# Kernel optimization log

Measured on AMD Instinct MI355X. Metric: run time of the kernel, lower is better.

The kernel has to match this reference:

```python
import jax, jax.numpy as jnp
import numpy as np

N_NODES = 100000
N_EDGES = 1600000
IN_DIM, HID_DIM, OUT_DIM = 256, 64, 64
EPS = 1e-12  # F.normalize eps


def _gcn_conv(x, src, dst, norm, W, b, num_nodes):
    # PyG-style GCNConv: transform, then symmetric-normalized aggregation.
    h = x @ W                                   # [N, d_out]
    msg = norm[:, None] * h[src]                # [E+N, d_out] gathered messages
    out = jax.ops.segment_sum(msg, dst, num_segments=num_nodes)
    return out + b


def _l2_normalize(h):
    # F.normalize(h, p=2, dim=1)
    n = jnp.sqrt(jnp.sum(h * h, axis=-1, keepdims=True))
    return h / jnp.maximum(n, EPS)


def setup_inputs() -> dict:
    key = jax.random.key(0)
    ks = jax.random.split(key, 8)
    x = jax.random.normal(ks[0], (N_NODES, IN_DIM), dtype=jnp.float32)
    edge_index = jax.random.randint(ks[1], (2, N_EDGES), 0, N_NODES, dtype=jnp.int64)
    def glorot(k, fan_in, fan_out):
        s = np.sqrt(6.0 / (fan_in + fan_out)).astype(np.float32)
        return jax.random.uniform(k, (fan_in, fan_out), jnp.float32, -s, s)
    W1 = glorot(ks[2], IN_DIM, HID_DIM)
    W2 = glorot(ks[3], HID_DIM, HID_DIM)
    W3 = glorot(ks[4], HID_DIM, OUT_DIM)
    b1 = jnp.zeros((HID_DIM,), jnp.float32)
    b2 = jnp.zeros((HID_DIM,), jnp.float32)
    b3 = jnp.zeros((OUT_DIM,), jnp.float32)
    return {"x": x, "edge_index": edge_index,
            "W1": W1, "b1": b1, "W2": W2, "b2": b2, "W3": W3, "b3": b3}


def reference(x, edge_index, W1, b1, W2, b2, W3, b3):
    N = x.shape[0]
    # add self-loops and compute symmetric norm D^-1/2 A_hat D^-1/2
    loop = jnp.arange(N, dtype=edge_index.dtype)
    src = jnp.concatenate([edge_index[0], loop])
    dst = jnp.concatenate([edge_index[1], loop])
    deg = jax.ops.segment_sum(jnp.ones_like(src, dtype=x.dtype), dst, num_segments=N)
    dinv = jnp.where(deg > 0, jax.lax.rsqrt(jnp.maximum(deg, 1.0)), 0.0)
    norm = dinv[src] * dinv[dst]                # [E+N]

    # layer 1: conv -> relu -> (dropout p=0 = identity) -> L2-normalize
    h = jax.nn.relu(_gcn_conv(x, src, dst, norm, W1, b1, N))
    h = _l2_normalize(h)
    # layer 2
    h = jax.nn.relu(_gcn_conv(h, src, dst, norm, W2, b2, N))
    h = _l2_normalize(h)
    # final layer: plain conv (cast to float32, already float32)
    out = _gcn_conv(h, src, dst, norm, W3, b3, N)
    return out
```

## Files before the change

kernel.cpp:

```cpp
#include <hip/hip_runtime.h>
#include <hip/hip_bf16.h>
#include <math.h>

#define HID 64
#define KT 64

#define NBBITS 10
#define NBSZ 1024
#define P1_BMAX 128
#define P1_CH 4096
#define P1_CAP 96

static inline size_t align256(size_t x) { return (x + 255) & ~(size_t)255; }

__device__ inline void gld_lds16(const float* g, float* lds) {
  __builtin_amdgcn_global_load_lds((const __attribute__((address_space(1))) void*)g,
                                   (__attribute__((address_space(3))) void*)lds, 16, 0, 0);
}


__global__ void count_dst_kernel(const int* __restrict__ dst, int* __restrict__ cnt, int E) {
  int e = blockIdx.x * blockDim.x + threadIdx.x;
  if (e < E) atomicAdd(&cnt[dst[e]], 1);
}

__global__ void dinv_kernel(const int* __restrict__ cnt, float* __restrict__ dinv, int N) {
  int i = blockIdx.x * blockDim.x + threadIdx.x;
  if (i < N) dinv[i] = rsqrtf((float)(cnt[i] + 1));
}


__global__ void bucket_count_kernel(const int* __restrict__ dst, int* __restrict__ bcnt,
                                    int E, int B) {
  __shared__ int sh[1024];
  for (int i = threadIdx.x; i < B; i += blockDim.x) sh[i] = 0;
  __syncthreads();
  for (int e = blockIdx.x * blockDim.x + threadIdx.x; e < E; e += gridDim.x * blockDim.x)
    atomicAdd(&sh[dst[e] >> NBBITS], 1);
  __syncthreads();
  for (int i = threadIdx.x; i < B; i += blockDim.x) {
    int v = sh[i];
    if (v) atomicAdd(&bcnt[i], v);
  }
}

__global__ __launch_bounds__(1024) void bucket_scan_kernel(const int* __restrict__ bcnt,
                                                           int* __restrict__ bbase,
                                                           int* __restrict__ gcur, int B) {
  __shared__ int sh[1024];
  int t = threadIdx.x;
  int v = (t < B) ? bcnt[t] : 0;
  sh[t] = v;
  __syncthreads();
  for (int off = 1; off < 1024; off <<= 1) {
    int u = (t >= off) ? sh[t - off] : 0;
    __syncthreads();
    sh[t] += u;
    __syncthreads();
  }
  if (t < B) {
    int ex = sh[t] - v;
    bbase[t] = ex;
    gcur[t] = ex;
  }
  if (t == 1023) bbase[B] = sh[1023];
}

__global__ __launch_bounds__(256) void bucketize_kernel(const int* __restrict__ src,
                                                        const int* __restrict__ dst,
                                                        int* __restrict__ gcur,
                                                        int* __restrict__ ebuck, int E) {
  __shared__ int cnt[P1_BMAX];
  __shared__ int lists[P1_BMAX * P1_CAP];
  int t = threadIdx.x;
  for (int i = t; i < P1_BMAX; i += 256) cnt[i] = 0;
  __syncthreads();
  int base_e = blockIdx.x * P1_CH;
#pragma unroll
  for (int u = 0; u < P1_CH / 256; ++u) {
    int e = base_e + u * 256 + t;
    if (e < E) {
      int s = src[e], d = dst[e];
      int bk = d >> NBBITS;
      int packed = (s << NBBITS) | (d & (NBSZ - 1));
      int p = atomicAdd(&cnt[bk], 1);
      if (p < P1_CAP) {
        lists[bk * P1_CAP + p] = packed;
      } else {
        int gp = atomicAdd(&gcur[bk], 1);
        ebuck[gp] = packed;
      }
    }
  }
  __syncthreads();
  int w = t >> 6, lane = t & 63;
  int bk = w * 32 + (lane & 31);
  int c = min(cnt[bk], P1_CAP);
  int mybase = 0;
  if (lane < 32 && c > 0) mybase = atomicAdd(&gcur[bk], c);
#pragma unroll 1
  for (int i = 0; i < 32; ++i) {
    int cb = __shfl(c, i);
    if (cb == 0) continue;
    int gb = __shfl(mybase, i);
    int bb = w * 32 + i;
    if (lane < cb) ebuck[gb + lane] = lists[bb * P1_CAP + lane];
    if (cb > 64 && lane < cb - 64) ebuck[gb + 64 + lane] = lists[bb * P1_CAP + 64 + lane];
  }
}

__global__ __launch_bounds__(1024) void bucket_sort_kernel(const int* __restrict__ ebuck,
                                                           const int* __restrict__ bbase,
                                                           int* __restrict__ rowptr,
                                                           int* __restrict__ epack,
                                                           int N, int B, int E) {
  __shared__ int lcnt[NBSZ];
  __shared__ int lcur[NBSZ];
  int b = blockIdx.x;
  int t = threadIdx.x;
  int n0 = b << NBBITS;
  lcnt[t] = 0;
  __syncthreads();
  int e0 = bbase[b], e1 = bbase[b + 1];
  for (int i = e0 + t; i < e1; i += 1024) atomicAdd(&lcnt[ebuck[i] & (NBSZ - 1)], 1);
  __syncthreads();
  int v = lcnt[t];
  for (int off = 1; off < 1024; off <<= 1) {
    int u = (t >= off) ? lcnt[t - off] : 0;
    __syncthreads();
    lcnt[t] += u;
    __syncthreads();
  }
  int ex = lcnt[t] - v;
  int node = n0 + t;
  if (node < N) rowptr[node] = e0 + ex;
  if (b == B - 1 && t == 0) rowptr[N] = E;
  lcur[t] = e0 + ex;
  __syncthreads();
  for (int i = e0 + t; i < e1; i += 1024) {
    int pv = ebuck[i];
    int pos = atomicAdd(&lcur[pv & (NBSZ - 1)], 1);
    epack[pos] = ((unsigned)pv) >> NBBITS;
  }
}

__global__ void dinv_rowptr_kernel(const int* __restrict__ rowptr, float* __restrict__ dinv,
                                   int N) {
  int i = blockIdx.x * blockDim.x + threadIdx.x;
  if (i < N) dinv[i] = rsqrtf((float)(rowptr[i + 1] - rowptr[i] + 1));
}


template <int K, typename OT>
__global__ __launch_bounds__(256, 4) void gemm_kernel(const float* __restrict__ x,
                                                      const float* __restrict__ W,
                                                      OT* __restrict__ out, int N) {
  __shared__ float Xs[64 * KT];
  __shared__ float Ws[KT * 64];
  const int t = threadIdx.x;
  const int lane = t & 63;
  const int w = t >> 6;
  const int rg = lane >> 4;
  const int cg = lane & 15;
  const int row0 = blockIdx.x * 64;
  float4 acc[4];
#pragma unroll
  for (int r = 0; r < 4; ++r) acc[r] = make_float4(0.f, 0.f, 0.f, 0.f);

  for (int k0 = 0; k0 < K; k0 += KT) {
    if (k0) __syncthreads();
    const float* Wg = W + (size_t)k0 * HID;
#pragma unroll
    for (int c = 0; c < 4; ++c) {
      int idx = c * 256 + t;
      gld_lds16(Wg + idx * 4, &Ws[idx * 4]);
      int srow = idx >> 4;
      int sg = (idx & 15) ^ ((srow >> 2) & 3);
      int grow = min(row0 + srow, N - 1);
      gld_lds16(x + (size_t)grow * K + k0 + (sg << 2), &Xs[idx * 4]);
    }
    __syncthreads();
    const int rbase = w * 16 + rg * 4;
#pragma unroll 4
    for (int kb = 0; kb < KT / 4; ++kb) {
      float4 wq0 = *(const float4*)&Ws[(4 * kb + 0) * HID + cg * 4];
      float4 wq1 = *(const float4*)&Ws[(4 * kb + 1) * HID + cg * 4];
      float4 wq2 = *(const float4*)&Ws[(4 * kb + 2) * HID + cg * 4];
      float4 wq3 = *(const float4*)&Ws[(4 * kb + 3) * HID + cg * 4];
      const int sg = (kb ^ rg) << 2;
#pragma unroll
      for (int r = 0; r < 4; ++r) {
        float4 xv = *(const float4*)&Xs[(rbase + r) * KT + sg];
        acc[r].x = fmaf(xv.w, wq3.x, fmaf(xv.z, wq2.x, fmaf(xv.y, wq1.x, fmaf(xv.x, wq0.x, acc[r].x))));
        acc[r].y = fmaf(xv.w, wq3.y, fmaf(xv.z, wq2.y, fmaf(xv.y, wq1.y, fmaf(xv.x, wq0.y, acc[r].y))));
        acc[r].z = fmaf(xv.w, wq3.z, fmaf(xv.z, wq2.z, fmaf(xv.y, wq1.z, fmaf(xv.x, wq0.z, acc[r].z))));
        acc[r].w = fmaf(xv.w, wq3.w, fmaf(xv.z, wq2.w, fmaf(xv.y, wq1.w, fmaf(xv.x, wq0.w, acc[r].w))));
      }
    }
  }
#pragma unroll
  for (int r = 0; r < 4; ++r) {
    int row = row0 + w * 16 + rg * 4 + r;
    if (row < N) {
      OT* o = out + (size_t)row * HID + cg * 4;
      o[0] = (OT)acc[r].x; o[1] = (OT)acc[r].y; o[2] = (OT)acc[r].z; o[3] = (OT)acc[r].w;
    }
  }
}


__device__ inline float bf_lo(unsigned int u) { return __uint_as_float(u << 16); }
__device__ inline float bf_hi(unsigned int u) { return __uint_as_float(u & 0xffff0000u); }

template <bool RELU_NORM>
__global__ void agg_kernel(const int* __restrict__ rowptr, const int* __restrict__ ep,
                           const float* __restrict__ dinv, const uint2* __restrict__ h64,
                           const float* __restrict__ bias, float* __restrict__ out, int N) {
  int grp = (blockIdx.x * blockDim.x + threadIdx.x) >> 6;
  int lane = threadIdx.x & 63;
  int q = lane >> 4;
  int sub = lane & 15;
  int node = grp * 4 + q;
  if (node >= N) return;
  int beg = rowptr[node];
  int end = rowptr[node + 1];
  float di = dinv[node];
  float dd = di * di;
  uint2 su = h64[(size_t)node * 16 + sub];
  float4 b4 = *(const float4*)&bias[sub * 4];
  float a0 = dd * bf_lo(su.x) + b4.x;
  float a1 = dd * bf_hi(su.x) + b4.y;
  float a2 = dd * bf_lo(su.y) + b4.z;
  float a3 = dd * bf_hi(su.y) + b4.w;
  int j = beg;
  for (; j + 8 <= end; j += 8) {
    int e[8];
    float dv[8];
    uint2 hv[8];
#pragma unroll
    for (int u = 0; u < 8; ++u) e[u] = ep[j + u];
#pragma unroll
    for (int u = 0; u < 8; ++u) dv[u] = dinv[e[u]];
#pragma unroll
    for (int u = 0; u < 8; ++u) hv[u] = h64[(size_t)e[u] * 16 + sub];
#pragma unroll
    for (int u = 0; u < 8; ++u) {
      float wn = di * dv[u];
      a0 = fmaf(wn, bf_lo(hv[u].x), a0);
      a1 = fmaf(wn, bf_hi(hv[u].x), a1);
      a2 = fmaf(wn, bf_lo(hv[u].y), a2);
      a3 = fmaf(wn, bf_hi(hv[u].y), a3);
    }
  }
  for (; j < end; ++j) {
    int e0 = ep[j];
    float wn = di * dinv[e0];
    uint2 hu = h64[(size_t)e0 * 16 + sub];
    a0 = fmaf(wn, bf_lo(hu.x), a0);
    a1 = fmaf(wn, bf_hi(hu.x), a1);
    a2 = fmaf(wn, bf_lo(hu.y), a2);
    a3 = fmaf(wn, bf_hi(hu.y), a3);
  }
  float4 v;
  if (RELU_NORM) {
    v.x = fmaxf(a0, 0.f); v.y = fmaxf(a1, 0.f);
    v.z = fmaxf(a2, 0.f); v.w = fmaxf(a3, 0.f);
    float ss = v.x * v.x + v.y * v.y + v.z * v.z + v.w * v.w;
#pragma unroll
    for (int off = 8; off; off >>= 1) ss += __shfl_xor(ss, off, 64);
    float inv = 1.f / fmaxf(sqrtf(ss), 1e-12f);
    v.x *= inv; v.y *= inv; v.z *= inv; v.w *= inv;
  } else {
    v = make_float4(a0, a1, a2, a3);
  }
  *(float4*)&out[(size_t)node * HID + sub * 4] = v;
}


__global__ void init_agg_kernel(const float* __restrict__ dinv, const float* __restrict__ h,
                                const float* __restrict__ bias, float* __restrict__ out, int N) {
  int t = blockIdx.x * blockDim.x + threadIdx.x;
  int i = t >> 6, f = t & 63;
  if (i >= N) return;
  float di = dinv[i];
  out[t] = di * di * h[t] + bias[f];
}

__global__ void edge_atomic_kernel(const int* __restrict__ src, const int* __restrict__ dst,
                                   const float* __restrict__ dinv, const float* __restrict__ h,
                                   float* __restrict__ out, int E) {
  int t = blockIdx.x * blockDim.x + threadIdx.x;
  int e = t >> 6;
  if (e >= E) return;
  int f = t & 63;
  int s = src[e], d = dst[e];
  atomicAdd(&out[(size_t)d * HID + f], dinv[s] * dinv[d] * h[(size_t)s * HID + f]);
}

__global__ void relu_norm_kernel(float* __restrict__ hbuf, int N) {
  int t = blockIdx.x * blockDim.x + threadIdx.x;
  int i = t >> 6;
  if (i >= N) return;
  float v = fmaxf(hbuf[t], 0.f);
  float ss = v * v;
#pragma unroll
  for (int off = 32; off; off >>= 1) ss += __shfl_xor(ss, off, 64);
  hbuf[t] = v / fmaxf(sqrtf(ss), 1e-12f);
}


extern "C" void kernel_launch(void* const* d_in, const int* in_sizes, int n_in,
                              void* d_out, int out_size, void* d_ws, size_t ws_size,
                              hipStream_t stream) {
  const float* x  = (const float*)d_in[0];
  const int*   ei = (const int*)d_in[1];
  const float* W1 = (const float*)d_in[2];
  const float* b1 = (const float*)d_in[3];
  const float* W2 = (const float*)d_in[4];
  const float* b2 = (const float*)d_in[5];
  const float* W3 = (const float*)d_in[6];
  const float* b3 = (const float*)d_in[7];
  float* out = (float*)d_out;

  const int IN = in_sizes[2] / HID;
  const int N  = in_sizes[0] / IN;
  const int E  = in_sizes[1] / 2;
  const int* srcI = ei;
  const int* dstI = ei + E;
  const int B = (N + NBSZ - 1) >> NBBITS;

  char* w = (char*)d_ws;
  size_t off = 0;
  auto alloc = [&](size_t bytes) { void* p = w + off; off = align256(off + bytes); return p; };
  float* A      = (float*)alloc((size_t)N * HID * 4);
  float* dinv   = (float*)alloc((size_t)N * 4);
  int*   cnt    = (int*)alloc((size_t)N * 4);
  size_t base_need = off;
  int*   rowptr = (int*)alloc((size_t)(N + 1) * 4);
  int*   epack  = (int*)alloc((size_t)E * 4);
  int*   bbase  = (int*)alloc(1032 * 4);
  int*   gcur   = (int*)alloc(1024 * 4);
  int*   bcnt   = (int*)alloc(1024 * 4);
  size_t csr_need = off;

  if (base_need > ws_size) return;
  const bool use_csr = (csr_need <= ws_size) && (B <= P1_BMAX) &&
                       ((size_t)E <= (size_t)N * HID) && (N <= (1 << 20));
  __hip_bfloat16* Ab = (__hip_bfloat16*)A;
  uint2* Ab64 = (uint2*)A;
  int* ebuck = (int*)A;

  const int blkE    = (E + 255) / 256;
  const int blkN    = (N + 255) / 256;
  const int blkRow  = (N + 63) / 64;
  const int blkWave = (N * 64 + 255) / 256;
  const int blkAgg  = ((size_t)((N + 3) / 4) * 64 + 255) / 256;
  const int blkEF   = ((size_t)E * 64 + 255) / 256;
  const int blkBkt  = (E + P1_CH - 1) / P1_CH;

  if (use_csr) {
    hipMemsetAsync(bcnt, 0, 1024 * 4, stream);
    bucket_count_kernel<<<256, 256, 0, stream>>>(dstI, bcnt, E, B);
    bucket_scan_kernel<<<1, 1024, 0, stream>>>(bcnt, bbase, gcur, B);
    bucketize_kernel<<<blkBkt, 256, 0, stream>>>(srcI, dstI, gcur, ebuck, E);
    bucket_sort_kernel<<<B, 1024, 0, stream>>>(ebuck, bbase, rowptr, epack, N, B, E);
    dinv_rowptr_kernel<<<blkN, 256, 0, stream>>>(rowptr, dinv, N);

    gemm_kernel<256><<<blkRow, 256, 0, stream>>>(x, W1, Ab, N);
    agg_kernel<true><<<blkAgg, 256, 0, stream>>>(rowptr, epack, dinv, Ab64, b1, out, N);
    gemm_kernel<64><<<blkRow, 256, 0, stream>>>(out, W2, Ab, N);
    agg_kernel<true><<<blkAgg, 256, 0, stream>>>(rowptr, epack, dinv, Ab64, b2, out, N);
    gemm_kernel<64><<<blkRow, 256, 0, stream>>>(out, W3, Ab, N);
    agg_kernel<false><<<blkAgg, 256, 0, stream>>>(rowptr, epack, dinv, Ab64, b3, out, N);
  } else {
    hipMemsetAsync(cnt, 0, (size_t)N * 4, stream);
    count_dst_kernel<<<blkE, 256, 0, stream>>>(dstI, cnt, E);
    dinv_kernel<<<blkN, 256, 0, stream>>>(cnt, dinv, N);

    gemm_kernel<256><<<blkRow, 256, 0, stream>>>(x, W1, A, N);
    init_agg_kernel<<<blkWave, 256, 0, stream>>>(dinv, A, b1, out, N);
    edge_atomic_kernel<<<blkEF, 256, 0, stream>>>(srcI, dstI, dinv, A, out, E);
    relu_norm_kernel<<<blkWave, 256, 0, stream>>>(out, N);

    gemm_kernel<64><<<blkRow, 256, 0, stream>>>(out, W2, A, N);
    init_agg_kernel<<<blkWave, 256, 0, stream>>>(dinv, A, b2, out, N);
    edge_atomic_kernel<<<blkEF, 256, 0, stream>>>(srcI, dstI, dinv, A, out, E);
    relu_norm_kernel<<<blkWave, 256, 0, stream>>>(out, N);

    gemm_kernel<64><<<blkRow, 256, 0, stream>>>(out, W3, A, N);
    init_agg_kernel<<<blkWave, 256, 0, stream>>>(dinv, A, b3, out, N);
    edge_atomic_kernel<<<blkEF, 256, 0, stream>>>(srcI, dstI, dinv, A, out, E);
  }
}
```

Baseline: 416.4 us.

## Use split-bf16 MFMA GEMMs and fold source dinv scaling into GEMM output

Replaces the FP32 FMA GEMM with an MFMA bf16 kernel that emulates fp32 precision by splitting X and W into high and low bf16 parts (three MFMAs per tile). Weights are pre-split and laid out for MFMA by a small prep kernel. The GEMM epilogue scales each row by dinv[src], so aggregation no longer gathers dinv per edge and just sums, applying dinv[dst] once. The separate dinv kernel is folded into the bucket sort. The cost is extra conversion work and the precision of the split-bf16 approximation.

```diff
diff --git a/kernel.cpp b/kernel.cpp
--- a/kernel.cpp
+++ b/kernel.cpp
@@ -11,12 +11,23 @@
 #define P1_CH 4096
 #define P1_CAP 96
 
+typedef __attribute__((ext_vector_type(8))) short s16x8;
+typedef __attribute__((ext_vector_type(4))) float f32x4;
+
 static inline size_t align256(size_t x) { return (x + 255) & ~(size_t)255; }
 
 __device__ inline void gld_lds16(const float* g, float* lds) {
   __builtin_amdgcn_global_load_lds((const __attribute__((address_space(1))) void*)g,
                                    (__attribute__((address_space(3))) void*)lds, 16, 0, 0);
 }
+
+__device__ inline unsigned short f2bf(float f) {
+  unsigned u = __float_as_uint(f);
+  return (unsigned short)((u + 0x7FFFu + ((u >> 16) & 1u)) >> 16);
+}
+__device__ inline float bf2f(unsigned short h) { return __uint_as_float(((unsigned)h) << 16); }
+__device__ inline float bf_lo(unsigned int u) { return __uint_as_float(u << 16); }
+__device__ inline float bf_hi(unsigned int u) { return __uint_as_float(u & 0xffff0000u); }
 
 
 __global__ void count_dst_kernel(const int* __restrict__ dst, int* __restrict__ cnt, int E) {
@@ -113,6 +124,7 @@
                                                            const int* __restrict__ bbase,
                                                            int* __restrict__ rowptr,
                                                            int* __restrict__ epack,
+                                                           float* __restrict__ dinv,
                                                            int N, int B, int E) {
   __shared__ int lcnt[NBSZ];
   __shared__ int lcur[NBSZ];
@@ -133,7 +145,10 @@
   }
   int ex = lcnt[t] - v;
   int node = n0 + t;
-  if (node < N) rowptr[node] = e0 + ex;
+  if (node < N) {
+    rowptr[node] = e0 + ex;
+    dinv[node] = rsqrtf((float)(v + 1));
+  }
   if (b == B - 1 && t == 0) rowptr[N] = E;
   lcur[t] = e0 + ex;
   __syncthreads();
@@ -144,10 +159,140 @@
   }
 }
 
-__global__ void dinv_rowptr_kernel(const int* __restrict__ rowptr, float* __restrict__ dinv,
-                                   int N) {
-  int i = blockIdx.x * blockDim.x + threadIdx.x;
-  if (i < N) dinv[i] = rsqrtf((float)(rowptr[i + 1] - rowptr[i] + 1));
+
+__global__ void wprep_kernel(const float* __restrict__ W1, const float* __restrict__ W2,
+                             const float* __restrict__ W3, unsigned short* __restrict__ W1h,
+                             unsigned short* __restrict__ W1l, unsigned short* __restrict__ W2h,
+                             unsigned short* __restrict__ W2l, unsigned short* __restrict__ W3h,
+                             unsigned short* __restrict__ W3l) {
+  int b = blockIdx.x, t = threadIdx.x;
+  const float* W;
+  unsigned short *Dh, *Dl;
+  int idx;
+  if (b < 64)      { W = W1; Dh = W1h; Dl = W1l; idx = b * 256 + t; }
+  else if (b < 80) { W = W2; Dh = W2h; Dl = W2l; idx = (b - 64) * 256 + t; }
+  else             { W = W3; Dh = W3h; Dl = W3l; idx = (b - 80) * 256 + t; }
+  int j = idx & 7, lane = (idx >> 3) & 63, ct = (idx >> 9) & 3, s = idx >> 11;
+  int k = s * 32 + ((lane >> 4) << 3) + j;
+  int col = ct * 16 + (lane & 15);
+  float f = W[k * HID + col];
+  unsigned short h = f2bf(f);
+  Dh[idx] = h;
+  Dl[idx] = f2bf(f - bf2f(h));
+}
+
+
+template <int K>
+__global__ __launch_bounds__(256, 4) void gemm_mfma_kernel(
+    const float* __restrict__ x, const unsigned short* __restrict__ Wh,
+    const unsigned short* __restrict__ Wl, const float* __restrict__ dinv,
+    unsigned short* __restrict__ out, int N) {
+  constexpr int NS = K / 32;
+  __shared__ float xs[2][64 * 32];
+  const int t = threadIdx.x, lane = t & 63, w = t >> 6;
+  const int g = lane >> 4, r15 = lane & 15;
+  const int row0 = blockIdx.x * 64;
+  const int arow = w * 16 + r15;
+  f32x4 acc[4];
+#pragma unroll
+  for (int ct = 0; ct < 4; ++ct) acc[ct] = (f32x4){0.f, 0.f, 0.f, 0.f};
+
+  auto stage = [&](int buf, int s) {
+#pragma unroll
+    for (int c = 0; c < 2; ++c) {
+      int idx = c * 256 + t;
+      int row = idx >> 3, gp = idx & 7;
+      int gs = gp ^ (row & 7);
+      int grow = min(row0 + row, N - 1);
+      gld_lds16(x + (size_t)grow * K + s * 32 + gs * 4, &xs[buf][idx * 4]);
+    }
+  };
+  stage(0, 0);
+  for (int s = 0; s < NS; ++s) {
+    __syncthreads();
+    if (s + 1 < NS) stage((s + 1) & 1, s + 1);
+    const float* xb = &xs[s & 1][arow * 32];
+    float4 xv0 = *(const float4*)&xb[((2 * g) ^ (arow & 7)) * 4];
+    float4 xv1 = *(const float4*)&xb[((2 * g + 1) ^ (arow & 7)) * 4];
+    float xf[8] = {xv0.x, xv0.y, xv0.z, xv0.w, xv1.x, xv1.y, xv1.z, xv1.w};
+    s16x8 xh, xl;
+#pragma unroll
+    for (int j = 0; j < 8; ++j) {
+      unsigned short hb = f2bf(xf[j]);
+      xh[j] = (short)hb;
+      xl[j] = (short)f2bf(xf[j] - bf2f(hb));
+    }
+#pragma unroll
+    for (int ct = 0; ct < 4; ++ct) {
+      size_t o = (((size_t)(s * 4 + ct)) * 64 + lane) * 8;
+      s16x8 wh = *(const s16x8*)&Wh[o];
+      s16x8 wl = *(const s16x8*)&Wl[o];
+      acc[ct] = __builtin_amdgcn_mfma_f32_16x16x32_bf16(wh, xh, acc[ct], 0, 0, 0);
+      acc[ct] = __builtin_amdgcn_mfma_f32_16x16x32_bf16(wl, xh, acc[ct], 0, 0, 0);
+      acc[ct] = __builtin_amdgcn_mfma_f32_16x16x32_bf16(wh, xl, acc[ct], 0, 0, 0);
+    }
+  }
+  int row = row0 + arow;
+  if (row < N) {
+    float di = dinv[row];
+    unsigned short* orow = out + (size_t)row * HID;
+#pragma unroll
+    for (int ct = 0; ct < 4; ++ct) {
+      unsigned p0 = (unsigned)f2bf(di * acc[ct][0]) | ((unsigned)f2bf(di * acc[ct][1]) << 16);
+      unsigned p1 = (unsigned)f2bf(di * acc[ct][2]) | ((unsigned)f2bf(di * acc[ct][3]) << 16);
+      *(uint2*)&orow[ct * 16 + g * 4] = make_uint2(p0, p1);
+    }
+  }
+}
+
+
+template <bool RELU_NORM>
+__global__ void agg_kernel(const int* __restrict__ rowptr, const int* __restrict__ ep,
+                           const float* __restrict__ dinv, const uint2* __restrict__ h64,
+                           const float* __restrict__ bias, float* __restrict__ out, int N) {
+  int grp = (blockIdx.x * blockDim.x + threadIdx.x) >> 6;
+  int lane = threadIdx.x & 63;
+  int q = lane >> 4;
+  int sub = lane & 15;
+  int node = grp * 4 + q;
+  if (node >= N) return;
+  int beg = rowptr[node];
+  int end = rowptr[node + 1];
+  uint2 su = h64[(size_t)node * 16 + sub];
+  float a0 = bf_lo(su.x), a1 = bf_hi(su.x), a2 = bf_lo(su.y), a3 = bf_hi(su.y);
+  int j = beg;
+  for (; j + 8 <= end; j += 8) {
+    int e[8];
+    uint2 hv[8];
+#pragma unroll
+    for (int u = 0; u < 8; ++u) e[u] = ep[j + u];
+#pragma unroll
+    for (int u = 0; u < 8; ++u) hv[u] = h64[(size_t)e[u] * 16 + sub];
+#pragma unroll
+    for (int u = 0; u < 8; ++u) {
+      a0 += bf_lo(hv[u].x); a1 += bf_hi(hv[u].x);
+      a2 += bf_lo(hv[u].y); a3 += bf_hi(hv[u].y);
+    }
+  }
+  for (; j < end; ++j) {
+    uint2 hu = h64[(size_t)ep[j] * 16 + sub];
+    a0 += bf_lo(hu.x); a1 += bf_hi(hu.x); a2 += bf_lo(hu.y); a3 += bf_hi(hu.y);
+  }
+  float di = dinv[node];
+  float4 b4 = *(const float4*)&bias[sub * 4];
+  float4 v;
+  v.x = fmaf(di, a0, b4.x); v.y = fmaf(di, a1, b4.y);
+  v.z = fmaf(di, a2, b4.z); v.w = fmaf(di, a3, b4.w);
+  if (RELU_NORM) {
+    v.x = fmaxf(v.x, 0.f); v.y = fmaxf(v.y, 0.f);
+    v.z = fmaxf(v.z, 0.f); v.w = fmaxf(v.w, 0.f);
+    float ss = v.x * v.x + v.y * v.y + v.z * v.z + v.w * v.w;
+#pragma unroll
+    for (int off = 8; off; off >>= 1) ss += __shfl_xor(ss, off, 64);
+    float inv = 1.f / fmaxf(sqrtf(ss), 1e-12f);
+    v.x *= inv; v.y *= inv; v.z *= inv; v.w *= inv;
+  }
+  *(float4*)&out[(size_t)node * HID + sub * 4] = v;
 }
 
 
@@ -209,74 +354,6 @@
 }
 
 
-__device__ inline float bf_lo(unsigned int u) { return __uint_as_float(u << 16); }
-__device__ inline float bf_hi(unsigned int u) { return __uint_as_float(u & 0xffff0000u); }
-
-template <bool RELU_NORM>
-__global__ void agg_kernel(const int* __restrict__ rowptr, const int* __restrict__ ep,
-                           const float* __restrict__ dinv, const uint2* __restrict__ h64,
-                           const float* __restrict__ bias, float* __restrict__ out, int N) {
-  int grp = (blockIdx.x * blockDim.x + threadIdx.x) >> 6;
-  int lane = threadIdx.x & 63;
-  int q = lane >> 4;
-  int sub = lane & 15;
-  int node = grp * 4 + q;
-  if (node >= N) return;
-  int beg = rowptr[node];
-  int end = rowptr[node + 1];
-  float di = dinv[node];
-  float dd = di * di;
-  uint2 su = h64[(size_t)node * 16 + sub];
-  float4 b4 = *(const float4*)&bias[sub * 4];
-  float a0 = dd * bf_lo(su.x) + b4.x;
-  float a1 = dd * bf_hi(su.x) + b4.y;
-  float a2 = dd * bf_lo(su.y) + b4.z;
-  float a3 = dd * bf_hi(su.y) + b4.w;
-  int j = beg;
-  for (; j + 8 <= end; j += 8) {
-    int e[8];
-    float dv[8];
-    uint2 hv[8];
-#pragma unroll
-    for (int u = 0; u < 8; ++u) e[u] = ep[j + u];
-#pragma unroll
-    for (int u = 0; u < 8; ++u) dv[u] = dinv[e[u]];
-#pragma unroll
-    for (int u = 0; u < 8; ++u) hv[u] = h64[(size_t)e[u] * 16 + sub];
-#pragma unroll
-    for (int u = 0; u < 8; ++u) {
-      float wn = di * dv[u];
-      a0 = fmaf(wn, bf_lo(hv[u].x), a0);
-      a1 = fmaf(wn, bf_hi(hv[u].x), a1);
-      a2 = fmaf(wn, bf_lo(hv[u].y), a2);
-      a3 = fmaf(wn, bf_hi(hv[u].y), a3);
-    }
-  }
-  for (; j < end; ++j) {
-    int e0 = ep[j];
-    float wn = di * dinv[e0];
-    uint2 hu = h64[(size_t)e0 * 16 + sub];
-    a0 = fmaf(wn, bf_lo(hu.x), a0);
-    a1 = fmaf(wn, bf_hi(hu.x), a1);
-    a2 = fmaf(wn, bf_lo(hu.y), a2);
-    a3 = fmaf(wn, bf_hi(hu.y), a3);
-  }
-  float4 v;
-  if (RELU_NORM) {
-    v.x = fmaxf(a0, 0.f); v.y = fmaxf(a1, 0.f);
-    v.z = fmaxf(a2, 0.f); v.w = fmaxf(a3, 0.f);
-    float ss = v.x * v.x + v.y * v.y + v.z * v.z + v.w * v.w;
-#pragma unroll
-    for (int off = 8; off; off >>= 1) ss += __shfl_xor(ss, off, 64);
-    float inv = 1.f / fmaxf(sqrtf(ss), 1e-12f);
-    v.x *= inv; v.y *= inv; v.z *= inv; v.w *= inv;
-  } else {
-    v = make_float4(a0, a1, a2, a3);
-  }
-  *(float4*)&out[(size_t)node * HID + sub * 4] = v;
-}
-
-
 __global__ void init_agg_kernel(const float* __restrict__ dinv, const float* __restrict__ h,
                                 const float* __restrict__ bias, float* __restrict__ out, int N) {
   int t = blockIdx.x * blockDim.x + threadIdx.x;
@@ -341,13 +418,19 @@
   int*   bbase  = (int*)alloc(1032 * 4);
   int*   gcur   = (int*)alloc(1024 * 4);
   int*   bcnt   = (int*)alloc(1024 * 4);
+  unsigned short* W1h = (unsigned short*)alloc(16384 * 2);
+  unsigned short* W1l = (unsigned short*)alloc(16384 * 2);
+  unsigned short* W2h = (unsigned short*)alloc(4096 * 2);
+  unsigned short* W2l = (unsigned short*)alloc(4096 * 2);
+  unsigned short* W3h = (unsigned short*)alloc(4096 * 2);
+  unsigned short* W3l = (unsigned short*)alloc(4096 * 2);
   size_t csr_need = off;
 
   if (base_need > ws_size) return;
   const bool use_csr = (csr_need <= ws_size) && (B <= P1_BMAX) &&
                        ((size_t)E <= (size_t)N * HID) && (N <= (1 << 20));
-  __hip_bfloat16* Ab = (__hip_bfloat16*)A;
   uint2* Ab64 = (uint2*)A;
+  unsigned short* Abs = (unsigned short*)A;
   int* ebuck = (int*)A;
 
   const int blkE    = (E + 255) / 256;
@@ -360,17 +443,17 @@
 
   if (use_csr) {
     hipMemsetAsync(bcnt, 0, 1024 * 4, stream);
+    wprep_kernel<<<96, 256, 0, stream>>>(W1, W2, W3, W1h, W1l, W2h, W2l, W3h, W3l);
     bucket_count_kernel<<<256, 256, 0, stream>>>(dstI, bcnt, E, B);
     bucket_scan_kernel<<<1, 1024, 0, stream>>>(bcnt, bbase, gcur, B);
     bucketize_kernel<<<blkBkt, 256, 0, stream>>>(srcI, dstI, gcur, ebuck, E);
-    bucket_sort_kernel<<<B, 1024, 0, stream>>>(ebuck, bbase, rowptr, epack, N, B, E);
-    dinv_rowptr_kernel<<<blkN, 256, 0, stream>>>(rowptr, dinv, N);
-
-    gemm_kernel<256><<<blkRow, 256, 0, stream>>>(x, W1, Ab, N);
+    bucket_sort_kernel<<<B, 1024, 0, stream>>>(ebuck, bbase, rowptr, epack, dinv, N, B, E);
+
+    gemm_mfma_kernel<256><<<blkRow, 256, 0, stream>>>(x, W1h, W1l, dinv, Abs, N);
     agg_kernel<true><<<blkAgg, 256, 0, stream>>>(rowptr, epack, dinv, Ab64, b1, out, N);
-    gemm_kernel<64><<<blkRow, 256, 0, stream>>>(out, W2, Ab, N);
+    gemm_mfma_kernel<64><<<blkRow, 256, 0, stream>>>(out, W2h, W2l, dinv, Abs, N);
     agg_kernel<true><<<blkAgg, 256, 0, stream>>>(rowptr, epack, dinv, Ab64, b2, out, N);
-    gemm_kernel<64><<<blkRow, 256, 0, stream>>>(out, W3, Ab, N);
+    gemm_mfma_kernel<64><<<blkRow, 256, 0, stream>>>(out, W3h, W3l, dinv, Abs, N);
     agg_kernel<false><<<blkAgg, 256, 0, stream>>>(rowptr, epack, dinv, Ab64, b3, out, N);
   } else {
     hipMemsetAsync(cnt, 0, (size_t)N * 4, stream);
```

Result: faster. 387.2 us (-7.0%).
